# Kernel tuning notes

Hardware: AMD Instinct MI355X
Metric: run time of the kernel (lower is better)

Reference implementation:

```python
import jax, jax.numpy as jnp
import numpy as np
from jax import lax

T, I, H, L = 4096, 101, 1000, 4  # seq len, letters_num, hidden, num_layers


def setup_inputs() -> dict:
    key = jax.random.key(0)
    ks = jax.random.split(key, 9)
    s = 0.03  # weight scale ~ 1/sqrt(H)
    return {
        "x": jax.random.normal(ks[0], (T, 1, I), jnp.float32),
        "enc_Wih": jax.random.normal(ks[1], (L, 4 * H, I), jnp.float32) * s,
        "enc_Whh": jax.random.normal(ks[2], (L, 4 * H, H), jnp.float32) * s,
        "enc_bih": jax.random.normal(ks[3], (L, 4 * H), jnp.float32) * s,
        "enc_bhh": jax.random.normal(ks[4], (L, 4 * H), jnp.float32) * s,
        "dec_Wih": jax.random.normal(ks[5], (L, 4 * I, H), jnp.float32) * s,
        "dec_Whh": jax.random.normal(ks[6], (L, 4 * I, I), jnp.float32) * s,
        "dec_bih": jax.random.normal(ks[7], (L, 4 * I), jnp.float32) * s,
        "dec_bhh": jax.random.normal(ks[8], (L, 4 * I), jnp.float32) * s,
        "length": T,
    }


def _lstm_cell(x, h, c, Wih, Whh, bih, bhh):
    # PyTorch LSTMCell gate order: i, f, g, o
    gates = x @ Wih.T + bih + h @ Whh.T + bhh  # [T, 4*Hout]
    i, f, g, o = jnp.split(gates, 4, axis=-1)
    c = jax.nn.sigmoid(f) * c + jax.nn.sigmoid(i) * jnp.tanh(g)
    h = jax.nn.sigmoid(o) * jnp.tanh(c)
    return h, c


def _stack(xt, Wih, Whh, bih, bhh, hout):
    # Hidden is reset per timestep in the original, so timesteps are a batch;
    # only the layer chain is sequential. Every layer consumes the same xt.
    t = xt.shape[0]
    init = (jnp.zeros((t, hout), xt.dtype), jnp.zeros((t, hout), xt.dtype))

    def body(carry, p):
        h, c = carry
        wih, whh, bi, bh = p
        h, c = _lstm_cell(xt, h, c, wih, whh, bi, bh)
        return (h, c), None

    (h, _), _ = lax.scan(body, init, (Wih, Whh, bih, bhh))
    return h


def reference(x, enc_Wih, enc_Whh, enc_bih, enc_bhh,
              dec_Wih, dec_Whh, dec_bih, dec_bhh, length):
    xt = x[:, 0, :]                      # [T, I]
    hdim = enc_Whh.shape[-1]
    odim = dec_Whh.shape[-1]
    enc = jax.nn.relu(_stack(xt, enc_Wih, enc_Whh, enc_bih, enc_bhh, hdim))  # [T, H]
    dec = _stack(enc, dec_Wih, dec_Whh, dec_bih, dec_bhh, odim)              # [T, O]
    out = jax.nn.log_softmax(dec, axis=-1)[:, None, :]                       # [T, 1, O]
    return out
```

## Files before the change

### kernel.cpp

```cpp
#include <hip/hip_runtime.h>
#include <cstdint>
#include <cstddef>
#include <cmath>

typedef __bf16 bf16_t;
typedef __bf16 bf16x8 __attribute__((ext_vector_type(8)));
typedef float floatx4 __attribute__((ext_vector_type(4)));

#define AS1 __attribute__((address_space(1)))
#define AS3 __attribute__((address_space(3)))

__device__ __forceinline__ void gload_lds16(const bf16_t* g, bf16_t* l) {
    __builtin_amdgcn_global_load_lds((AS1 void*)(uintptr_t)(g), (AS3 void*)(l), 16, 0, 0);
}

__device__ __forceinline__ float sigf(float x) { return 1.0f / (1.0f + __expf(-x)); }
__device__ __forceinline__ float tanhfast(float x) { return 1.0f - 2.0f / (__expf(2.0f * x) + 1.0f); }

template<int BM>
__global__ __launch_bounds__(256, 4)
void gemm_lstm(const bf16_t* __restrict__ A, const bf16_t* __restrict__ B,
               const float* __restrict__ bias, float* __restrict__ c, int EP,
               bf16_t* __restrict__ hb, int ldH, int hoff, float* __restrict__ hf,
               int K, int ldA, int ldB, int relu, int czero)
{
    constexpr int AI = BM / 32;
    __shared__ bf16_t As[BM * 64];
    __shared__ bf16_t Bs[128 * 64];
    const int tid  = threadIdx.x;
    const int lane = tid & 63;
    const int w    = tid >> 6;
    const int wm   = (w & 1) * (BM / 2);
    const int wn   = (w >> 1) * 64;
    const int m0   = blockIdx.y * BM;
    const int n0   = blockIdx.x * 128;

    floatx4 zero = {0.0f, 0.0f, 0.0f, 0.0f};
    floatx4 acc[AI][4];
#pragma unroll
    for (int i = 0; i < AI; ++i)
#pragma unroll
        for (int j = 0; j < 4; ++j) acc[i][j] = zero;

    const int srow = lane >> 3;
    const int sk   = ((lane & 7) ^ srow) * 8;
    const int fr   = lane & 15;
    const int fx   = fr & 7;

    const bf16_t* Ag = A + (size_t)(m0 + srow) * ldA + sk;
    const bf16_t* Bg = B + (size_t)(n0 + srow) * ldB + sk;

    for (int k0 = 0; k0 < K; k0 += 64) {
        __syncthreads();
#pragma unroll
        for (int j = 0; j < AI; ++j) {
            int r0 = (w * AI + j) * 8;
            gload_lds16(Ag + (size_t)r0 * ldA + k0, As + r0 * 64 + lane * 8);
        }
#pragma unroll
        for (int j = 0; j < 4; ++j) {
            int r0 = (w * 4 + j) * 8;
            gload_lds16(Bg + (size_t)r0 * ldB + k0, Bs + r0 * 64 + lane * 8);
        }
        __syncthreads();
#pragma unroll
        for (int kk = 0; kk < 64; kk += 32) {
            const int pc = ((((kk >> 3) + (lane >> 4)) ^ fx) << 3);
            bf16x8 af[AI], bfr[4];
#pragma unroll
            for (int i = 0; i < AI; ++i)
                af[i] = *(const bf16x8*)(As + (wm + i * 16 + fr) * 64 + pc);
#pragma unroll
            for (int j = 0; j < 4; ++j)
                bfr[j] = *(const bf16x8*)(Bs + (wn + j * 16 + fr) * 64 + pc);
#pragma unroll
            for (int i = 0; i < AI; ++i)
#pragma unroll
                for (int j = 0; j < 4; ++j)
                    acc[i][j] = __builtin_amdgcn_mfma_f32_16x16x32_bf16(af[i], bfr[j], acc[i][j], 0, 0, 0);
        }
    }

    const int crow = (lane >> 4) * 4;
    const int ccol = lane & 15;
    const int e    = ((n0 + wn) >> 2) + ccol;
    float bi[4];
#pragma unroll
    for (int j = 0; j < 4; ++j) bi[j] = bias[n0 + wn + j * 16 + ccol];

#pragma unroll
    for (int i = 0; i < AI; ++i) {
#pragma unroll
        for (int r = 0; r < 4; ++r) {
            int t = m0 + wm + i * 16 + crow + r;
            float iv = acc[i][0][r] + bi[0];
            float fv = acc[i][1][r] + bi[1];
            float gv = acc[i][2][r] + bi[2];
            float ov = acc[i][3][r] + bi[3];
            size_t cix = (size_t)t * EP + e;
            float cold = 0.0f;
            if (!czero) cold = c[cix];
            float cv = sigf(fv) * cold + sigf(iv) * tanhfast(gv);
            c[cix] = cv;
            float hv = sigf(ov) * tanhfast(cv);
            if (relu) hv = fmaxf(hv, 0.0f);
            if (hb) hb[(size_t)t * ldH + hoff + e] = (bf16_t)hv;
            else    hf[(size_t)t * EP + e] = hv;
        }
    }
}

__global__ void pack_all(const float* __restrict__ x,
                         const float* __restrict__ eWih, const float* __restrict__ eWhh,
                         const float* __restrict__ ebih, const float* __restrict__ ebhh,
                         const float* __restrict__ dWih, const float* __restrict__ dWhh,
                         const float* __restrict__ dbih, const float* __restrict__ dbhh,
                         bf16_t* __restrict__ Aenc, bf16_t* __restrict__ Wenc,
                         bf16_t* __restrict__ Wdec,
                         float* __restrict__ bse, float* __restrict__ bsd)
{
    const int b = blockIdx.x;
    if (b < 9216) {
        int gid = b * 256 + threadIdx.x;
        int row = gid / 144, grp = gid - row * 144;
        int l = row >> 12, p = row & 4095;
        int g = (p >> 4) & 3, e = ((p >> 6) << 4) + (p & 15);
        int c0 = grp * 8;
        float v[8];
#pragma unroll
        for (int u = 0; u < 8; ++u) v[u] = 0.0f;
        if (e < 1000) {
            size_t r = (size_t)l * 4000 + g * 1000 + e;
            if (c0 >= 128 && c0 < 1128) {
                const float* src = eWhh + r * 1000 + (c0 - 128);
                float4 a = *(const float4*)src;
                float4 bq = *(const float4*)(src + 4);
                v[0]=a.x; v[1]=a.y; v[2]=a.z; v[3]=a.w; v[4]=bq.x; v[5]=bq.y; v[6]=bq.z; v[7]=bq.w;
            } else if (c0 < 128) {
                const float* src = eWih + r * 101;
#pragma unroll
                for (int u = 0; u < 8; ++u) { int cc = c0 + u; if (cc < 101) v[u] = src[cc]; }
            }
        }
        bf16x8 o;
#pragma unroll
        for (int u = 0; u < 8; ++u) o[u] = (bf16_t)v[u];
        *(bf16x8*)(Wenc + (size_t)row * 1152 + c0) = o;
    } else if (b < 11520) {
        int gid = (b - 9216) * 256 + threadIdx.x;
        int row = gid / 144, grp = gid - row * 144;
        int c0  = grp * 8;
        float v[8];
#pragma unroll
        for (int u = 0; u < 8; ++u) v[u] = 0.0f;
        if (c0 < 101) {
            const float* src = x + (size_t)row * 101;
#pragma unroll
            for (int u = 0; u < 8; ++u) { int cc = c0 + u; if (cc < 101) v[u] = src[cc]; }
        }
        bf16x8 o;
#pragma unroll
        for (int u = 0; u < 8; ++u) o[u] = (bf16_t)v[u];
        *(bf16x8*)(Aenc + (size_t)row * 1152 + c0) = o;
    } else if (b < 12672) {
        int gid = (b - 11520) * 256 + threadIdx.x;
        int row = gid / 144, grp = gid - row * 144;
        int l = row >> 9, p = row & 511;
        int g = (p >> 4) & 3, e = ((p >> 6) << 4) + (p & 15);
        int c0 = grp * 8;
        float v[8];
#pragma unroll
        for (int u = 0; u < 8; ++u) v[u] = 0.0f;
        if (e < 101) {
            size_t r = (size_t)l * 404 + g * 101 + e;
            if (c0 < 1000) {
                const float* src = dWih + r * 1000 + c0;
                float4 a = *(const float4*)src;
                float4 bq = *(const float4*)(src + 4);
                v[0]=a.x; v[1]=a.y; v[2]=a.z; v[3]=a.w; v[4]=bq.x; v[5]=bq.y; v[6]=bq.z; v[7]=bq.w;
            } else if (c0 >= 1024 && c0 < 1128) {
                const float* src = dWhh + r * 101;
#pragma unroll
                for (int u = 0; u < 8; ++u) { int cc = c0 + u; if (cc < 1125) v[u] = src[cc - 1024]; }
            }
        }
        bf16x8 o;
#pragma unroll
        for (int u = 0; u < 8; ++u) o[u] = (bf16_t)v[u];
        *(bf16x8*)(Wdec + (size_t)row * 1152 + c0) = o;
    } else {
        int idx = (b - 12672) * 256 + threadIdx.x;
        if (idx < 16384) {
            int l = idx >> 12, p = idx & 4095;
            int g = (p >> 4) & 3, e = ((p >> 6) << 4) + (p & 15);
            bse[idx] = (e < 1000) ? (ebih[l * 4000 + g * 1000 + e] + ebhh[l * 4000 + g * 1000 + e]) : 0.0f;
        } else {
            int k = idx - 16384;
            int l = k >> 9, p = k & 511;
            int g = (p >> 4) & 3, e = ((p >> 6) << 4) + (p & 15);
            bsd[k] = (e < 101) ? (dbih[l * 404 + g * 101 + e] + dbhh[l * 404 + g * 101 + e]) : 0.0f;
        }
    }
}

__global__ void log_softmax_k(const float* __restrict__ h, float* __restrict__ out)
{
    int row = blockIdx.x;
    int l   = threadIdx.x;
    const float* hr = h + (size_t)row * 128;
    float v1 = (l < 101)      ? hr[l]      : -INFINITY;
    float v2 = (l + 64 < 101) ? hr[l + 64] : -INFINITY;
    float m = fmaxf(v1, v2);
#pragma unroll
    for (int off = 32; off > 0; off >>= 1) m = fmaxf(m, __shfl_down(m, off));
    m = __shfl(m, 0);
    float ev = ((l < 101) ? __expf(v1 - m) : 0.0f) + ((l + 64 < 101) ? __expf(v2 - m) : 0.0f);
#pragma unroll
    for (int off = 32; off > 0; off >>= 1) ev += __shfl_down(ev, off);
    float lse = m + __logf(__shfl(ev, 0));
    float* orow = out + (size_t)row * 101;
    if (l < 101)      orow[l]      = v1 - lse;
    if (l + 64 < 101) orow[l + 64] = v2 - lse;
}

extern "C" void kernel_launch(void* const* d_in, const int* in_sizes, int n_in,
                              void* d_out, int out_size, void* d_ws, size_t ws_size,
                              hipStream_t stream)
{
    (void)in_sizes; (void)n_in; (void)out_size; (void)ws_size;
    const float* x    = (const float*)d_in[0];
    const float* eWih = (const float*)d_in[1];
    const float* eWhh = (const float*)d_in[2];
    const float* ebih = (const float*)d_in[3];
    const float* ebhh = (const float*)d_in[4];
    const float* dWih = (const float*)d_in[5];
    const float* dWhh = (const float*)d_in[6];
    const float* dbih = (const float*)d_in[7];
    const float* dbhh = (const float*)d_in[8];

    char* ws = (char*)d_ws;
    bf16_t* Aenc = (bf16_t*)(ws);
    bf16_t* Wenc = (bf16_t*)(ws + 9437184);
    bf16_t* Adec = (bf16_t*)(ws + 47185920);
    bf16_t* Wdec = (bf16_t*)(ws + 56623104);
    float*  bse  = (float*) (ws + 61341696);
    float*  bsd  = (float*) (ws + 61407232);
    float*  cenc = (float*) (ws + 61415424);
    float*  cdec = (float*) (ws + 78192640);
    float*  hdec = (float*) (ws + 80289792);

    pack_all<<<12744, 256, 0, stream>>>(x, eWih, eWhh, ebih, ebhh, dWih, dWhh, dbih, dbhh,
                                        Aenc, Wenc, Wdec, bse, bsd);

    for (int l = 0; l < 4; ++l) {
        gemm_lstm<128><<<dim3(32, 32), 256, 0, stream>>>(
            Aenc, Wenc + (size_t)l * 4096 * 1152, bse + l * 4096,
            cenc, 1024,
            (l < 3) ? Aenc : Adec, 1152, (l < 3) ? 128 : 0, nullptr,
            (l == 0) ? 128 : 1152, 1152, 1152, (l == 3) ? 1 : 0, (l == 0) ? 1 : 0);
    }
    for (int l = 0; l < 4; ++l) {
        gemm_lstm<32><<<dim3(4, 128), 256, 0, stream>>>(
            Adec, Wdec + (size_t)l * 512 * 1152, bsd + l * 512,
            cdec, 128,
            (l < 3) ? Adec : nullptr, 1152, 1024, (l == 3) ? hdec : nullptr,
            (l == 0) ? 1024 : 1152, 1152, 1152, 0, (l == 0) ? 1 : 0);
    }
    log_softmax_k<<<4096, 64, 0, stream>>>(hdec, (float*)d_out);
}
```

Measured before the change: 354.0 us.

## Use 256x256-tile 8-wave GEMM with multi-stage LDS pipeline for encoder layers

Adds a new encoder GEMM+LSTM kernel with 512 threads, 256x256 output tiles, a 4-slot LDS ring buffer staged with async global-to-LDS loads, and explicit vmcnt/barrier scheduling so loads overlap MFMA work. It also swizzles the block index for L2 locality and raises MFMA priority. The goal is to cut load latency stalls and improve operand reuse in the large encoder GEMMs. In exchange it launches only 256 blocks, which is about one wave on the device, and it relies on hand-tuned wait counts that are fragile if K does not fit the assumed pattern.

```diff
diff --git a/kernel.cpp b/kernel.cpp
--- a/kernel.cpp
+++ b/kernel.cpp
@@ -17,69 +17,92 @@
 __device__ __forceinline__ float sigf(float x) { return 1.0f / (1.0f + __expf(-x)); }
 __device__ __forceinline__ float tanhfast(float x) { return 1.0f - 2.0f / (__expf(2.0f * x) + 1.0f); }
 
-template<int BM>
-__global__ __launch_bounds__(256, 4)
-void gemm_lstm(const bf16_t* __restrict__ A, const bf16_t* __restrict__ B,
-               const float* __restrict__ bias, float* __restrict__ c, int EP,
-               bf16_t* __restrict__ hb, int ldH, int hoff, float* __restrict__ hf,
-               int K, int ldA, int ldB, int relu, int czero)
-{
-    constexpr int AI = BM / 32;
-    __shared__ bf16_t As[BM * 64];
-    __shared__ bf16_t Bs[128 * 64];
+__global__ __launch_bounds__(512, 2)
+void gemm_lstm8(const bf16_t* __restrict__ A, const bf16_t* __restrict__ Bw,
+                const float* __restrict__ bias, float* __restrict__ c, int EP,
+                bf16_t* __restrict__ hb, int ldH, int hoff, float* __restrict__ hf,
+                int K, int ldA, int ldB, int relu, int czero)
+{
+    __shared__ bf16_t As[4 * 8192];
+    __shared__ bf16_t Bs[4 * 8192];
     const int tid  = threadIdx.x;
     const int lane = tid & 63;
     const int w    = tid >> 6;
-    const int wm   = (w & 1) * (BM / 2);
+    const int wm   = (w & 1) * 128;
     const int wn   = (w >> 1) * 64;
-    const int m0   = blockIdx.y * BM;
-    const int n0   = blockIdx.x * 128;
+
+    const int bid = blockIdx.x;
+    const int swz = (bid & 7) * 32 + (bid >> 3);
+    const int m0  = (swz & 15) * 256;
+    const int n0  = (swz >> 4) * 256;
+
+    const int NT = K >> 6;
+
+    const int srow = tid >> 2;
+    const int slc  = (tid & 3) ^ ((tid >> 3) & 3);
+    const bf16_t* Asrc0 = A  + (size_t)(m0 + srow) * ldA + slc * 8;
+    const bf16_t* Asrc1 = Asrc0 + (size_t)128 * ldA;
+    const bf16_t* Bsrc0 = Bw + (size_t)(n0 + srow) * ldB + slc * 8;
+    const bf16_t* Bsrc1 = Bsrc0 + (size_t)128 * ldB;
+    bf16_t* AsD = As + tid * 8;
+    bf16_t* BsD = Bs + tid * 8;
+
+    const int fr    = lane & 15;
+    const int rdoff = fr * 32 + (((lane >> 4) ^ ((fr >> 1) & 3)) * 8);
 
     floatx4 zero = {0.0f, 0.0f, 0.0f, 0.0f};
-    floatx4 acc[AI][4];
-#pragma unroll
-    for (int i = 0; i < AI; ++i)
+    floatx4 acc[8][4];
+#pragma unroll
+    for (int i = 0; i < 8; ++i)
 #pragma unroll
         for (int j = 0; j < 4; ++j) acc[i][j] = zero;
-
-    const int srow = lane >> 3;
-    const int sk   = ((lane & 7) ^ srow) * 8;
-    const int fr   = lane & 15;
-    const int fx   = fr & 7;
-
-    const bf16_t* Ag = A + (size_t)(m0 + srow) * ldA + sk;
-    const bf16_t* Bg = B + (size_t)(n0 + srow) * ldB + sk;
-
-    for (int k0 = 0; k0 < K; k0 += 64) {
-        __syncthreads();
-#pragma unroll
-        for (int j = 0; j < AI; ++j) {
-            int r0 = (w * AI + j) * 8;
-            gload_lds16(Ag + (size_t)r0 * ldA + k0, As + r0 * 64 + lane * 8);
-        }
-#pragma unroll
-        for (int j = 0; j < 4; ++j) {
-            int r0 = (w * 4 + j) * 8;
-            gload_lds16(Bg + (size_t)r0 * ldB + k0, Bs + r0 * 64 + lane * 8);
-        }
-        __syncthreads();
-#pragma unroll
-        for (int kk = 0; kk < 64; kk += 32) {
-            const int pc = ((((kk >> 3) + (lane >> 4)) ^ fx) << 3);
-            bf16x8 af[AI], bfr[4];
-#pragma unroll
-            for (int i = 0; i < AI; ++i)
-                af[i] = *(const bf16x8*)(As + (wm + i * 16 + fr) * 64 + pc);
-#pragma unroll
-            for (int j = 0; j < 4; ++j)
-                bfr[j] = *(const bf16x8*)(Bs + (wn + j * 16 + fr) * 64 + pc);
-#pragma unroll
-            for (int i = 0; i < AI; ++i)
-#pragma unroll
-                for (int j = 0; j < 4; ++j)
-                    acc[i][j] = __builtin_amdgcn_mfma_f32_16x16x32_bf16(af[i], bfr[j], acc[i][j], 0, 0, 0);
-        }
-    }
+    bf16x8 af[4], bfr[4];
+
+#define STAGE_A8(slot, koff) { gload_lds16(Asrc0 + (koff), AsD + (slot) * 8192); \
+                               gload_lds16(Asrc1 + (koff), AsD + (slot) * 8192 + 4096); }
+#define STAGE_B8(slot, koff) { gload_lds16(Bsrc0 + (koff), BsD + (slot) * 8192); \
+                               gload_lds16(Bsrc1 + (koff), BsD + (slot) * 8192 + 4096); }
+#define RD_B8(slot) { _Pragma("unroll") for (int j = 0; j < 4; ++j) \
+    bfr[j] = *(const bf16x8*)(Bs + (slot) * 8192 + (wn + j * 16) * 32 + rdoff); }
+#define RD_A8(slot, ib) { _Pragma("unroll") for (int ii = 0; ii < 4; ++ii) \
+    af[ii] = *(const bf16x8*)(As + (slot) * 8192 + (wm + ((ib) + ii) * 16) * 32 + rdoff); }
+#define MF8(ib) { __builtin_amdgcn_s_setprio(1); \
+    _Pragma("unroll") for (int ii = 0; ii < 4; ++ii) \
+    _Pragma("unroll") for (int j = 0; j < 4; ++j) \
+        acc[(ib) + ii][j] = __builtin_amdgcn_mfma_f32_16x16x32_bf16(af[ii], bfr[j], acc[(ib) + ii][j], 0, 0, 0); \
+    __builtin_amdgcn_s_setprio(0); }
+#define BAR8()  __builtin_amdgcn_s_barrier()
+#define LGKM0() asm volatile("s_waitcnt lgkmcnt(0)" ::: "memory")
+
+    STAGE_A8(0, 0);  STAGE_B8(0, 0);
+    STAGE_A8(1, 32); STAGE_B8(1, 32);
+    STAGE_A8(2, 64); STAGE_B8(2, 64);
+    asm volatile("s_waitcnt vmcnt(8)" ::: "memory");
+    BAR8();
+
+#define TILE8(t, doS01, doS23, VM1, VM3)                                   \
+  { const int sA0 = (2 * (t)) & 3, sA1 = (2 * (t) + 1) & 3;                \
+    const int sN  = (2 * (t) + 3) & 3;                                     \
+    const int kN1 = ((t) + 1) * 64 + 32, kN2 = ((t) + 2) * 64;             \
+    RD_B8(sA0); RD_A8(sA0, 0);                                             \
+    if (doS01) STAGE_A8(sN, kN1);                                          \
+    BAR8(); LGKM0(); MF8(0); BAR8();                                       \
+    RD_A8(sA0, 4);                                                         \
+    if (doS01) STAGE_B8(sN, kN1);                                          \
+    BAR8(); LGKM0(); MF8(4);                                               \
+    asm volatile("s_waitcnt " VM1 ::: "memory"); BAR8();                   \
+    RD_B8(sA1); RD_A8(sA1, 0);                                             \
+    if (doS23) STAGE_A8(sA0, kN2);                                         \
+    BAR8(); LGKM0(); MF8(0); BAR8();                                       \
+    RD_A8(sA1, 4);                                                         \
+    if (doS23) STAGE_B8(sA0, kN2);                                         \
+    BAR8(); LGKM0(); MF8(4);                                               \
+    asm volatile("s_waitcnt " VM3 ::: "memory"); BAR8(); }
+
+    for (int t = 0; t + 2 < NT; ++t)
+        TILE8(t, 1, 1, "vmcnt(8)", "vmcnt(8)");
+    TILE8(NT - 2, 1, 0, "vmcnt(8)", "vmcnt(4)");
+    TILE8(NT - 1, 0, 0, "vmcnt(0)", "vmcnt(0)");
 
     const int crow = (lane >> 4) * 4;
     const int ccol = lane & 15;
@@ -89,7 +112,7 @@
     for (int j = 0; j < 4; ++j) bi[j] = bias[n0 + wn + j * 16 + ccol];
 
 #pragma unroll
-    for (int i = 0; i < AI; ++i) {
+    for (int i = 0; i < 8; ++i) {
 #pragma unroll
         for (int r = 0; r < 4; ++r) {
             int t = m0 + wm + i * 16 + crow + r;
@@ -110,6 +133,99 @@
     }
 }
 
+template<int BM>
+__global__ __launch_bounds__(256, 4)
+void gemm_lstm(const bf16_t* __restrict__ A, const bf16_t* __restrict__ B,
+               const float* __restrict__ bias, float* __restrict__ c, int EP,
+               bf16_t* __restrict__ hb, int ldH, int hoff, float* __restrict__ hf,
+               int K, int ldA, int ldB, int relu, int czero)
+{
+    constexpr int AI = BM / 32;
+    __shared__ bf16_t As[BM * 64];
+    __shared__ bf16_t Bs[128 * 64];
+    const int tid  = threadIdx.x;
+    const int lane = tid & 63;
+    const int w    = tid >> 6;
+    const int wm   = (w & 1) * (BM / 2);
+    const int wn   = (w >> 1) * 64;
+    const int m0   = blockIdx.y * BM;
+    const int n0   = blockIdx.x * 128;
+
+    floatx4 zero = {0.0f, 0.0f, 0.0f, 0.0f};
+    floatx4 acc[AI][4];
+#pragma unroll
+    for (int i = 0; i < AI; ++i)
+#pragma unroll
+        for (int j = 0; j < 4; ++j) acc[i][j] = zero;
+
+    const int srow = lane >> 3;
+    const int sk   = ((lane & 7) ^ srow) * 8;
+    const int fr   = lane & 15;
+    const int fx   = fr & 7;
+
+    const bf16_t* Ag = A + (size_t)(m0 + srow) * ldA + sk;
+    const bf16_t* Bg = B + (size_t)(n0 + srow) * ldB + sk;
+
+    for (int k0 = 0; k0 < K; k0 += 64) {
+        __syncthreads();
+#pragma unroll
+        for (int j = 0; j < AI; ++j) {
+            int r0 = (w * AI + j) * 8;
+            gload_lds16(Ag + (size_t)r0 * ldA + k0, As + r0 * 64 + lane * 8);
+        }
+#pragma unroll
+        for (int j = 0; j < 4; ++j) {
+            int r0 = (w * 4 + j) * 8;
+            gload_lds16(Bg + (size_t)r0 * ldB + k0, Bs + r0 * 64 + lane * 8);
+        }
+        __syncthreads();
+#pragma unroll
+        for (int kk = 0; kk < 64; kk += 32) {
+            const int pc = ((((kk >> 3) + (lane >> 4)) ^ fx) << 3);
+            bf16x8 af[AI], bfr[4];
+#pragma unroll
+            for (int i = 0; i < AI; ++i)
+                af[i] = *(const bf16x8*)(As + (wm + i * 16 + fr) * 64 + pc);
+#pragma unroll
+            for (int j = 0; j < 4; ++j)
+                bfr[j] = *(const bf16x8*)(Bs + (wn + j * 16 + fr) * 64 + pc);
+#pragma unroll
+            for (int i = 0; i < AI; ++i)
+#pragma unroll
+                for (int j = 0; j < 4; ++j)
+                    acc[i][j] = __builtin_amdgcn_mfma_f32_16x16x32_bf16(af[i], bfr[j], acc[i][j], 0, 0, 0);
+        }
+    }
+
+    const int crow = (lane >> 4) * 4;
+    const int ccol = lane & 15;
+    const int e    = ((n0 + wn) >> 2) + ccol;
+    float bi[4];
+#pragma unroll
+    for (int j = 0; j < 4; ++j) bi[j] = bias[n0 + wn + j * 16 + ccol];
+
+#pragma unroll
+    for (int i = 0; i < AI; ++i) {
+#pragma unroll
+        for (int r = 0; r < 4; ++r) {
+            int t = m0 + wm + i * 16 + crow + r;
+            float iv = acc[i][0][r] + bi[0];
+            float fv = acc[i][1][r] + bi[1];
+            float gv = acc[i][2][r] + bi[2];
+            float ov = acc[i][3][r] + bi[3];
+            size_t cix = (size_t)t * EP + e;
+            float cold = 0.0f;
+            if (!czero) cold = c[cix];
+            float cv = sigf(fv) * cold + sigf(iv) * tanhfast(gv);
+            c[cix] = cv;
+            float hv = sigf(ov) * tanhfast(cv);
+            if (relu) hv = fmaxf(hv, 0.0f);
+            if (hb) hb[(size_t)t * ldH + hoff + e] = (bf16_t)hv;
+            else    hf[(size_t)t * EP + e] = hv;
+        }
+    }
+}
+
 __global__ void pack_all(const float* __restrict__ x,
                          const float* __restrict__ eWih, const float* __restrict__ eWhh,
                          const float* __restrict__ ebih, const float* __restrict__ ebhh,
@@ -253,7 +369,7 @@
                                         Aenc, Wenc, Wdec, bse, bsd);
 
     for (int l = 0; l < 4; ++l) {
-        gemm_lstm<128><<<dim3(32, 32), 256, 0, stream>>>(
+        gemm_lstm8<<<256, 512, 0, stream>>>(
             Aenc, Wenc + (size_t)l * 4096 * 1152, bse + l * 4096,
             cenc, 1024,
             (l < 3) ? Aenc : Adec, 1152, (l < 3) ? 128 : 0, nullptr,
```

Measured after the change: 371.6 us. 1.05x slower.
